# Performance work log

Measured on AMD Instinct MI355X. Metric: run time of the kernel, lower is better.

Reference implementation:

```python
import jax, jax.numpy as jnp
import numpy as np
import math

V, D, H, F, L, S, B = 50257, 1024, 16, 4096, 4, 2048, 2
DK = D // H

def setup_inputs() -> dict:
    key = jax.random.key(0)
    ks = iter(jax.random.split(key, 32))
    std = 0.02
    def nrm(shape):
        return (std * jax.random.normal(next(ks), shape)).astype(jnp.float32)
    inp = {
        "x": jax.random.randint(next(ks), (B, S), 0, V, dtype=jnp.int32),
        "emb": nrm((V, D)),
        "ln1_g": jnp.ones((L, D), jnp.float32), "ln1_b": jnp.zeros((L, D), jnp.float32),
        "wq": nrm((L, D, D)), "wk": nrm((L, D, D)), "wv": nrm((L, D, D)), "wo": nrm((L, D, D)),
        "ln2_g": jnp.ones((L, D), jnp.float32), "ln2_b": jnp.zeros((L, D), jnp.float32),
        "w1": nrm((L, D, F)), "b1": jnp.zeros((L, F), jnp.float32),
        "w2": nrm((L, F, D)), "b2": jnp.zeros((L, D), jnp.float32),
        "lnf_g": jnp.ones((D,), jnp.float32), "lnf_b": jnp.zeros((D,), jnp.float32),
        "head_w": nrm((D, V)), "head_b": jnp.zeros((V,), jnp.float32),
    }
    return inp

def _layernorm(x, g, b, eps=1e-5):
    mu = jnp.mean(x, axis=-1, keepdims=True)
    var = jnp.var(x, axis=-1, keepdims=True)
    return (x - mu) * jax.lax.rsqrt(var + eps) * g + b

def _posenc(seq_len, d_model, dtype):
    pos = jnp.arange(seq_len, dtype=jnp.float32)[:, None]                  # [S,1]
    div = jnp.exp(jnp.arange(0, d_model, 2, dtype=jnp.float32) * (-math.log(10000.0) / d_model))
    ang = pos * div                                                        # [S,D/2]
    pe = jnp.stack([jnp.sin(ang), jnp.cos(ang)], axis=-1).reshape(seq_len, d_model)
    return pe.astype(dtype)

def reference(x, emb, ln1_g, ln1_b, wq, wk, wv, wo, ln2_g, ln2_b, w1, b1, w2, b2, lnf_g, lnf_b, head_w, head_b):
    b, s = x.shape
    h = emb[x] + _posenc(s, D, emb.dtype)[None]                            # [B,S,D]
    causal = jnp.tril(jnp.ones((s, s), dtype=bool))                       # True = keep
    scale = 1.0 / math.sqrt(DK)
    neg_inf = jnp.finfo(h.dtype).min
    for l in range(L):
        # --- attention sublayer ---
        hn = _layernorm(h, ln1_g[l], ln1_b[l])
        q = (hn @ wq[l]).reshape(b, s, H, DK)
        k = (hn @ wk[l]).reshape(b, s, H, DK)
        v = (hn @ wv[l]).reshape(b, s, H, DK)
        scores = jnp.einsum("bqhd,bkhd->bhqk", q, k) * scale
        scores = jnp.where(causal[None, None], scores, neg_inf)
        w = jax.nn.softmax(scores, axis=-1)
        attn = jnp.einsum("bhqk,bkhd->bqhd", w, v).reshape(b, s, D)
        h = h + attn @ wo[l]
        # --- FFN sublayer ---
        hn = _layernorm(h, ln2_g[l], ln2_b[l])
        h = h + jax.nn.relu(hn @ w1[l] + b1[l]) @ w2[l] + b2[l]
    h = _layernorm(h, lnf_g, lnf_b)
    logits = h @ head_w + head_b                                           # [B,S,V]
    return logits
```

## Files before the change

kernel.cpp:

```cpp
#include <hip/hip_runtime.h>
#include <math.h>

#define VOCAB 50257
#define VPAD  50432
#define DM    1024
#define NH    16
#define DKH   64
#define FF    4096
#define NL    4
#define SEQ   2048
#define BATCH 2
#define MROWS (BATCH*SEQ)

typedef __bf16 bf16_t;
typedef __bf16 bf16x8 __attribute__((ext_vector_type(8)));
typedef __bf16 bf16x4 __attribute__((ext_vector_type(4)));
typedef float  f32x4  __attribute__((ext_vector_type(4)));

typedef void as1_void __attribute__((address_space(1)));
typedef void as3_void __attribute__((address_space(3)));

__device__ __forceinline__ void gload_lds16(const void* g, void* l) {
  __builtin_amdgcn_global_load_lds((as1_void*)g, (as3_void*)l, 16, 0, 0);
}

__device__ __forceinline__ uint32_t lds_addr32(const void* p) {
  return (uint32_t)(uintptr_t)(as3_void*)p;
}

__device__ __forceinline__ bf16x8 dsr128(uint32_t addr) {
  bf16x8 v;
  asm volatile("ds_read_b128 %0, %1" : "=v"(v) : "v"(addr));
  return v;
}

#define FENCE asm volatile("" ::: "memory")
#define BAR() do { FENCE; __builtin_amdgcn_s_barrier(); FENCE; } while (0)
#define LGKM0_FENCE() do { \
  asm volatile("s_waitcnt lgkmcnt(0)" ::: "memory"); \
  __builtin_amdgcn_sched_barrier(0); \
} while (0)

__global__ __launch_bounds__(256) void embed_kernel(const int* __restrict__ x,
    const float* __restrict__ emb, float* __restrict__ h) {
  int row = blockIdx.x;
  int s = row & (SEQ - 1);
  int d = threadIdx.x * 4;
  const float* e = emb + (size_t)x[row] * DM + d;
  float4 v = *(const float4*)e;
  float vin[4] = {v.x, v.y, v.z, v.w};
  float out[4];
#pragma unroll
  for (int j = 0; j < 4; ++j) {
    int dd = d + j;
    int i = dd >> 1;
    float freq = expf(-0.017988946039016376f * (float)i);
    float ang = (float)s * freq;
    float pe = (dd & 1) ? cosf(ang) : sinf(ang);
    out[j] = vin[j] + pe;
  }
  *(float4*)(h + (size_t)row * DM + d) = make_float4(out[0], out[1], out[2], out[3]);
}

__global__ __launch_bounds__(256) void ln_kernel(const float* __restrict__ x,
    const float* __restrict__ g, const float* __restrict__ b, bf16_t* __restrict__ out) {
  int row = blockIdx.x;
  int tid = threadIdx.x, lane = tid & 63, wave = tid >> 6;
  const float* xr = x + (size_t)row * DM;
  float4 v = ((const float4*)xr)[tid];
  float s1 = v.x + v.y + v.z + v.w;
  float s2 = v.x * v.x + v.y * v.y + v.z * v.z + v.w * v.w;
#pragma unroll
  for (int d = 1; d < 64; d <<= 1) { s1 += __shfl_xor(s1, d); s2 += __shfl_xor(s2, d); }
  __shared__ float red[8];
  if (lane == 0) { red[wave] = s1; red[4 + wave] = s2; }
  __syncthreads();
  s1 = red[0] + red[1] + red[2] + red[3];
  s2 = red[4] + red[5] + red[6] + red[7];
  float mu = s1 * (1.0f / DM);
  float var = s2 * (1.0f / DM) - mu * mu;
  float rs = rsqrtf(var + 1e-5f);
  float4 gv = ((const float4*)g)[tid];
  float4 bv = ((const float4*)b)[tid];
  bf16x4 o;
  o[0] = (bf16_t)((v.x - mu) * rs * gv.x + bv.x);
  o[1] = (bf16_t)((v.y - mu) * rs * gv.y + bv.y);
  o[2] = (bf16_t)((v.z - mu) * rs * gv.z + bv.z);
  o[3] = (bf16_t)((v.w - mu) * rs * gv.w + bv.w);
  *(bf16x4*)(out + (size_t)row * DM + tid * 4) = o;
}

__global__ __launch_bounds__(256) void transpose_cast_kernel(const float* __restrict__ in,
    bf16_t* __restrict__ out, int K, int N, int Npad) {
  __shared__ float tile[32][33];
  int n0 = blockIdx.x * 32, k0 = blockIdx.y * 32;
  int tx = threadIdx.x & 31, ty = threadIdx.x >> 5;
#pragma unroll
  for (int kk = ty; kk < 32; kk += 8) {
    int n = n0 + tx;
    tile[kk][tx] = (n < N) ? in[(size_t)(k0 + kk) * N + n] : 0.f;
  }
  __syncthreads();
#pragma unroll
  for (int nn = ty; nn < 32; nn += 8) {
    out[(size_t)(n0 + nn) * K + k0 + tx] = (bf16_t)tile[tx][nn];
  }
}

__global__ __launch_bounds__(256) void wtrans_kernel(
    const float* __restrict__ wq, const float* __restrict__ wk,
    const float* __restrict__ wv, const float* __restrict__ wo,
    const float* __restrict__ w1, const float* __restrict__ w2,
    bf16_t* __restrict__ qkvT, bf16_t* __restrict__ woT,
    bf16_t* __restrict__ w1T, bf16_t* __restrict__ w2T) {
  int id = blockIdx.x;
  const float* src; bf16_t* dst; int K, N, tk, tn;
  if (id < 4096) {
    int m = id >> 10, tile_i = id & 1023;
    tk = tile_i >> 5; tn = tile_i & 31; K = 1024; N = 1024;
    src = (m == 0) ? wq : (m == 1) ? wk : (m == 2) ? wv : wo;
    dst = (m < 3) ? qkvT + (size_t)m * DM * DM : woT;
  } else if (id < 8192) {
    int tile_i = id - 4096;
    tk = tile_i >> 7; tn = tile_i & 127; K = 1024; N = 4096;
    src = w1; dst = w1T;
  } else {
    int tile_i = id - 8192;
    tk = tile_i >> 5; tn = tile_i & 31; K = 4096; N = 1024;
    src = w2; dst = w2T;
  }
  __shared__ float tile[32][33];
  int n0 = tn * 32, k0 = tk * 32;
  int tx = threadIdx.x & 31, ty = threadIdx.x >> 5;
#pragma unroll
  for (int kk = ty; kk < 32; kk += 8)
    tile[kk][tx] = src[(size_t)(k0 + kk) * N + n0 + tx];
  __syncthreads();
#pragma unroll
  for (int nn = ty; nn < 32; nn += 8)
    dst[(size_t)(n0 + nn) * K + k0 + tx] = (bf16_t)tile[tx][nn];
}

__global__ __launch_bounds__(256) void vtrans_kernel(const bf16_t* __restrict__ qkv,
    bf16_t* __restrict__ vT) {
  int sb = blockIdx.x, hh = blockIdx.y, bb = blockIdx.z;
  __shared__ bf16_t t[64][72];
  int tid = threadIdx.x;
  const bf16_t* src = qkv + ((size_t)bb * SEQ + sb * 64) * (3 * DM) + 2 * DM + hh * DKH;
#pragma unroll
  for (int c = 0; c < 2; ++c) {
    int u = c * 256 + tid;
    int s = u >> 3, d8 = u & 7;
    *(bf16x8*)&t[s][d8 * 8] = *(const bf16x8*)(src + (size_t)s * (3 * DM) + d8 * 8);
  }
  __syncthreads();
  bf16_t* dst = vT + ((size_t)(bb * NH + hh) * DKH) * SEQ + sb * 64;
#pragma unroll
  for (int c = 0; c < 2; ++c) {
    int u = c * 256 + tid;
    int dk = u >> 3, s8 = u & 7;
    bf16x8 v;
#pragma unroll
    for (int j = 0; j < 8; ++j) v[j] = t[s8 * 8 + j][dk];
    *(bf16x8*)(dst + (size_t)dk * SEQ + s8 * 8) = v;
  }
}

__global__ __launch_bounds__(256, 2) void gemm128_kernel(
    const bf16_t* __restrict__ A, const bf16_t* __restrict__ Bt, int K,
    const float* __restrict__ bias, const float* __restrict__ Rsd,
    float* Cf, bf16_t* Cb, int ldc, int Nvalid, int relu, int gridM, int gridN) {
  __shared__ __align__(16) bf16_t lds[32768];

  int nwg = gridM * gridN;
  int orig = blockIdx.x;
  int q = nwg >> 3, rr = nwg & 7;
  int xcd = orig & 7, idx = orig >> 3;
  int swz = (xcd < rr ? xcd * (q + 1) : rr * (q + 1) + (xcd - rr) * q) + idx;
  int bm = swz % gridM, bn = swz / gridM;
  int m0 = bm * 128, n0 = bn * 128;

  int tid = threadIdx.x, lane = tid & 63, wave = tid >> 6;
  int g = lane >> 4, r = lane & 15;
  int wr = wave >> 1, wc = wave & 1;

  f32x4 zero = {0.f, 0.f, 0.f, 0.f};
  f32x4 acc[4][4];
#pragma unroll
  for (int i = 0; i < 4; ++i)
#pragma unroll
    for (int j = 0; j < 4; ++j) acc[i][j] = zero;

  const bf16_t* Abase = A + (size_t)m0 * K;
  const bf16_t* Bbase = Bt + (size_t)n0 * K;
  int NT = K >> 6;

  uint32_t L0 = lds_addr32(lds);
  uint32_t aF = L0 + (uint32_t)((g * 128 + wr * 64 + r) * 16);
  uint32_t bF = L0 + 32768u + (uint32_t)((g * 128 + wc * 64 + r) * 16);

  auto stage = [&](int t) {
    int b = t & 1, k0 = t << 6;
    bf16_t* dA = lds + (size_t)b * 8192;
    bf16_t* dB = lds + 16384 + (size_t)b * 8192;
#pragma unroll
    for (int j = 0; j < 4; ++j) {
      int u = j * 256 + tid;
      int row = u & 127, k8 = u >> 7;
      gload_lds16(Abase + (size_t)row * K + k0 + k8 * 8, dA + (j * 256 + wave * 64) * 8);
    }
#pragma unroll
    for (int j = 0; j < 4; ++j) {
      int u = j * 256 + tid;
      int row = u & 127, k8 = u >> 7;
      gload_lds16(Bbase + (size_t)row * K + k0 + k8 * 8, dB + (j * 256 + wave * 64) * 8);
    }
  };

  stage(0);
  if (NT > 1) {
    stage(1);
    asm volatile("s_waitcnt vmcnt(8)" ::: "memory");
  } else {
    asm volatile("s_waitcnt vmcnt(0)" ::: "memory");
  }
  BAR();

  for (int t = 0; t < NT; ++t) {
    uint32_t boff = (uint32_t)((t & 1) << 14);
    bf16x8 af[4][2], bfr[4][2];
#pragma unroll
    for (int mr = 0; mr < 4; ++mr)
#pragma unroll
      for (int kk = 0; kk < 2; ++kk)
        af[mr][kk] = dsr128(aF + boff + (uint32_t)(kk * 8192 + mr * 256));
#pragma unroll
    for (int nr = 0; nr < 4; ++nr)
#pragma unroll
      for (int kk = 0; kk < 2; ++kk)
        bfr[nr][kk] = dsr128(bF + boff + (uint32_t)(kk * 8192 + nr * 256));
    LGKM0_FENCE();
    BAR();
    if (t + 2 < NT) stage(t + 2);
    __builtin_amdgcn_s_setprio(1);
#pragma unroll
    for (int mr = 0; mr < 4; ++mr)
#pragma unroll
      for (int nr = 0; nr < 4; ++nr) {
        acc[mr][nr] = __builtin_amdgcn_mfma_f32_16x16x32_bf16(af[mr][0], bfr[nr][0], acc[mr][nr], 0, 0, 0);
        acc[mr][nr] = __builtin_amdgcn_mfma_f32_16x16x32_bf16(af[mr][1], bfr[nr][1], acc[mr][nr], 0, 0, 0);
      }
    __builtin_amdgcn_s_setprio(0);
    __builtin_amdgcn_sched_barrier(0);
    if (t + 2 < NT) {
      asm volatile("s_waitcnt vmcnt(8)" ::: "memory");
    } else {
      asm volatile("s_waitcnt vmcnt(0)" ::: "memory");
    }
    BAR();
  }

#pragma unroll
  for (int mr = 0; mr < 4; ++mr) {
    int row = m0 + wr * 64 + mr * 16 + g * 4;
#pragma unroll
    for (int nr = 0; nr < 4; ++nr) {
      int col = n0 + wc * 64 + nr * 16 + r;
      if (col < Nvalid) {
        float bval = bias ? bias[col] : 0.f;
#pragma unroll
        for (int i = 0; i < 4; ++i) {
          float vv = acc[mr][nr][i] + bval;
          if (relu) vv = fmaxf(vv, 0.f);
          size_t idxo = (size_t)(row + i) * ldc + col;
          if (Rsd) vv += Rsd[idxo];
          if (Cf) Cf[idxo] = vv;
          if (Cb) Cb[idxo] = (bf16_t)vv;
        }
      }
    }
  }
}

__global__ __launch_bounds__(512, 2) void gemm256_kernel(
    const bf16_t* __restrict__ A, const bf16_t* __restrict__ Bt, int K,
    const float* __restrict__ bias, float* Cf, bf16_t* Cb,
    int ldc, int Nvalid, int relu, int gridM, int gridN) {
  __shared__ __align__(16) bf16_t lds[65536];

  int nwg = gridM * gridN;
  int orig = blockIdx.x;
  int q = nwg >> 3, rr = nwg & 7;
  int xcd = orig & 7, idx = orig >> 3;
  int swz = (xcd < rr ? xcd * (q + 1) : rr * (q + 1) + (xcd - rr) * q) + idx;
  int bm = swz % gridM, bn = swz / gridM;
  int m0 = bm * 256, n0 = bn * 256;

  int tid = threadIdx.x, lane = tid & 63, wave = tid >> 6;
  int g = lane >> 4, r = lane & 15;
  int wr = wave >> 2, wc = wave & 3;

  f32x4 zero = {0.f, 0.f, 0.f, 0.f};
  f32x4 acc[8][4];
#pragma unroll
  for (int i = 0; i < 8; ++i)
#pragma unroll
    for (int j = 0; j < 4; ++j) acc[i][j] = zero;

  const bf16_t* Ab = A + (size_t)m0 * K;
  const bf16_t* Bb = Bt + (size_t)n0 * K;
  int NT = K >> 6;

  uint32_t L0 = lds_addr32(lds);
  uint32_t laneOff = (uint32_t)(g * 2048 + r * 16);
  uint32_t aBase0 = L0 + ((uint32_t)wr << 14) + laneOff;
  uint32_t bBase0 = L0 + 65536u + ((uint32_t)(wc >> 1) << 14) + laneOff
                  + (uint32_t)((wc & 1) * 1024);

  auto stageA = [&](int t, int hh) {
    int b = t & 1, k0 = t << 6;
    const bf16_t* src = Ab + (size_t)(hh * 128) * K + k0;
    bf16_t* dst = lds + (size_t)(b * 2 + hh) * 8192;
#pragma unroll
    for (int j = 0; j < 2; ++j) {
      int u = j * 512 + tid;
      gload_lds16(src + (size_t)(u & 127) * K + (u >> 7) * 8, dst + (j * 512 + wave * 64) * 8);
    }
  };
  auto stageB = [&](int t, int hh) {
    int b = t & 1, k0 = t << 6;
    const bf16_t* src = Bb + (size_t)(hh * 128) * K + k0;
    bf16_t* dst = lds + 32768 + (size_t)(b * 2 + hh) * 8192;
#pragma unroll
    for (int j = 0; j < 2; ++j) {
      int u = j * 512 + tid;
      gload_lds16(src + (size_t)(u & 127) * K + (u >> 7) * 8, dst + (j * 512 + wave * 64) * 8);
    }
  };

  stageB(0, 0); stageB(0, 1); stageA(0, 0); stageA(0, 1);
  if (NT > 1) {
    stageB(1, 0); stageB(1, 1);
    asm volatile("s_waitcnt vmcnt(4)" ::: "memory");
  } else {
    asm volatile("s_waitcnt vmcnt(0)" ::: "memory");
  }
  BAR();

  for (int t = 0; t < NT; ++t) {
    uint32_t bsel = (uint32_t)((t & 1) << 15);
    uint32_t Aaddr = aBase0 + bsel;
    uint32_t Baddr = bBase0 + bsel;

    bf16x8 a0[4][2], a1[4][2], b01[2][2], b23[2][2];

#pragma unroll
    for (int mi = 0; mi < 4; ++mi)
#pragma unroll
      for (int kk = 0; kk < 2; ++kk)
        a0[mi][kk] = dsr128(Aaddr + (uint32_t)(kk * 8192 + mi * 256));
#pragma unroll
    for (int ni = 0; ni < 2; ++ni)
#pragma unroll
      for (int kk = 0; kk < 2; ++kk)
        b01[ni][kk] = dsr128(Baddr + (uint32_t)(kk * 8192 + ni * 256));
    if (t + 1 < NT) stageA(t + 1, 0);
    BAR();
    LGKM0_FENCE();
    __builtin_amdgcn_s_setprio(1);
#pragma unroll
    for (int mi = 0; mi < 4; ++mi)
#pragma unroll
      for (int ni = 0; ni < 2; ++ni)
#pragma unroll
        for (int kk = 0; kk < 2; ++kk)
          acc[mi][ni] = __builtin_amdgcn_mfma_f32_16x16x32_bf16(a0[mi][kk], b01[ni][kk], acc[mi][ni], 0, 0, 0);
    __builtin_amdgcn_s_setprio(0);
    __builtin_amdgcn_sched_barrier(0);
    BAR();

#pragma unroll
    for (int ni = 0; ni < 2; ++ni)
#pragma unroll
      for (int kk = 0; kk < 2; ++kk)
        b23[ni][kk] = dsr128(Baddr + (uint32_t)(kk * 8192 + (ni + 2) * 256));
    if (t + 1 < NT) stageA(t + 1, 1);
    BAR();
    LGKM0_FENCE();
    __builtin_amdgcn_s_setprio(1);
#pragma unroll
    for (int mi = 0; mi < 4; ++mi)
#pragma unroll
      for (int ni = 0; ni < 2; ++ni)
#pragma unroll
        for (int kk = 0; kk < 2; ++kk)
          acc[mi][ni + 2] = __builtin_amdgcn_mfma_f32_16x16x32_bf16(a0[mi][kk], b23[ni][kk], acc[mi][ni + 2], 0, 0, 0);
    __builtin_amdgcn_s_setprio(0);
    __builtin_amdgcn_sched_barrier(0);
    BAR();

#pragma unroll
    for (int mi = 0; mi < 4; ++mi)
#pragma unroll
      for (int kk = 0; kk < 2; ++kk)
        a1[mi][kk] = dsr128(Aaddr + (uint32_t)(kk * 8192 + (mi + 4) * 256));
    if (t + 2 < NT) stageB(t + 2, 0);
    BAR();
    LGKM0_FENCE();
    __builtin_amdgcn_s_setprio(1);
#pragma unroll
    for (int mi = 0; mi < 4; ++mi)
#pragma unroll
      for (int ni = 0; ni < 2; ++ni)
#pragma unroll
        for (int kk = 0; kk < 2; ++kk)
          acc[mi + 4][ni] = __builtin_amdgcn_mfma_f32_16x16x32_bf16(a1[mi][kk], b01[ni][kk], acc[mi + 4][ni], 0, 0, 0);
    __builtin_amdgcn_s_setprio(0);
    __builtin_amdgcn_sched_barrier(0);
    BAR();

    if (t + 2 < NT) stageB(t + 2, 1);
    __builtin_amdgcn_sched_barrier(0);
    __builtin_amdgcn_s_setprio(1);
#pragma unroll
    for (int mi = 0; mi < 4; ++mi)
#pragma unroll
      for (int ni = 0; ni < 2; ++ni)
#pragma unroll
        for (int kk = 0; kk < 2; ++kk)
          acc[mi + 4][ni + 2] = __builtin_amdgcn_mfma_f32_16x16x32_bf16(a1[mi][kk], b23[ni][kk], acc[mi + 4][ni + 2], 0, 0, 0);
    __builtin_amdgcn_s_setprio(0);
    __builtin_amdgcn_sched_barrier(0);
    if (t + 2 < NT) {
      asm volatile("s_waitcnt vmcnt(4)" ::: "memory");
    } else {
      asm volatile("s_waitcnt vmcnt(0)" ::: "memory");
    }
    BAR();
  }

#pragma unroll
  for (int mi = 0; mi < 8; ++mi) {
    int row = m0 + wr * 128 + mi * 16 + g * 4;
#pragma unroll
    for (int ni = 0; ni < 4; ++ni) {
      int col = n0 + wc * 64 + ni * 16 + r;
      if (col < Nvalid) {
        float bval = bias ? bias[col] : 0.f;
#pragma unroll
        for (int i = 0; i < 4; ++i) {
          float vv = acc[mi][ni][i] + bval;
          if (relu) vv = fmaxf(vv, 0.f);
          size_t idxo = (size_t)(row + i) * ldc + col;
          if (Cf) Cf[idxo] = vv;
          if (Cb) Cb[idxo] = (bf16_t)vv;
        }
      }
    }
  }
}

__global__ __launch_bounds__(512, 4) void attn_kernel(const bf16_t* __restrict__ Qg,
    const bf16_t* __restrict__ Kg, const bf16_t* __restrict__ vT, bf16_t* __restrict__ Og,
    int ldq) {
  int bq = (int)gridDim.x - 1 - (int)blockIdx.x;
  int hh = blockIdx.y, bb = blockIdx.z;
  int tid = threadIdx.x, lane = tid & 63, wave = tid >> 6;
  int g = lane >> 4, r = lane & 15;
  __shared__ __align__(16) bf16_t Kl[2][4096];
  __shared__ __align__(16) bf16_t Vl[2][4096];
  __shared__ __align__(16) bf16_t Pl[8][1024];

  size_t base = (size_t)bb * SEQ * ldq + hh * DKH;
  size_t vbase = ((size_t)(bb * NH + hh)) * DKH * SEQ;
  size_t baseO = (size_t)bb * SEQ * DM + hh * DKH;
  int q0 = bq * 128 + wave * 16;
  const bf16_t* qrowp = Qg + base + (size_t)(q0 + r) * ldq;
  bf16x8 qf0 = *(const bf16x8*)(qrowp + g * 8);
  bf16x8 qf1 = *(const bf16x8*)(qrowp + 32 + g * 8);
#pragma unroll
  for (int j = 0; j < 8; ++j) {
    qf0[j] = (bf16_t)((float)qf0[j] * 0.125f);
    qf1[j] = (bf16_t)((float)qf1[j] * 0.125f);
  }

  uint32_t KlA = lds_addr32(&Kl[0][0]);
  uint32_t VlA = lds_addr32(&Vl[0][0]);
  int slot0 = g ^ (r & 7), slot1 = (4 + g) ^ (r & 7);

  f32x4 zero = {0.f, 0.f, 0.f, 0.f};
  f32x4 accO[4];
#pragma unroll
  for (int dt = 0; dt < 4; ++dt) accO[dt] = zero;
  float m_i[4], l_i[4];
#pragma unroll
  for (int i = 0; i < 4; ++i) { m_i[i] = -1e30f; l_i[i] = 0.f; }

  int skv = tid >> 3, kslot = tid & 7, kdk8 = kslot ^ (skv & 7);
  int sdk = tid >> 3, vslot = tid & 7, vkv8 = vslot ^ (sdk & 7);
  const bf16_t* ksrc0 = Kg + base + (size_t)skv * ldq + kdk8 * 8;
  const bf16_t* vsrc0 = vT + vbase + (size_t)sdk * SEQ + vkv8 * 8;

  auto stage = [&](int kb) {
    int c = kb & 1;
    gload_lds16(ksrc0 + (size_t)(kb * 64) * ldq, &Kl[c][(wave * 64) * 8]);
    gload_lds16(vsrc0 + kb * 64, &Vl[c][(wave * 64) * 8]);
  };

  int nkb = 2 * bq + 2;
  stage(0); stage(1);
  asm volatile("s_waitcnt vmcnt(2)" ::: "memory");
  BAR();

  for (int kb = 0; kb < nkb; ++kb) {
    uint32_t koff = KlA + (uint32_t)((kb & 1) << 13);
    uint32_t voff = VlA + (uint32_t)((kb & 1) << 13);

    bf16x8 kf[4][2];
#pragma unroll
    for (int ct = 0; ct < 4; ++ct) {
      int kvrow = ct * 16 + r;
      kf[ct][0] = dsr128(koff + (uint32_t)((kvrow * 8 + slot0) * 16));
      kf[ct][1] = dsr128(koff + (uint32_t)((kvrow * 8 + slot1) * 16));
    }
    LGKM0_FENCE();
    f32x4 sc[4];
#pragma unroll
    for (int ct = 0; ct < 4; ++ct) {
      f32x4 s = zero;
      s = __builtin_amdgcn_mfma_f32_16x16x32_bf16(qf0, kf[ct][0], s, 0, 0, 0);
      s = __builtin_amdgcn_mfma_f32_16x16x32_bf16(qf1, kf[ct][1], s, 0, 0, 0);
      sc[ct] = s;
    }

    bool full = (kb * 64 + 63) <= q0;
#pragma unroll
    for (int i = 0; i < 4; ++i) {
      float mx = m_i[i];
      if (full) {
#pragma unroll
        for (int ct = 0; ct < 4; ++ct) mx = fmaxf(mx, sc[ct][i]);
      } else {
        int qglob = q0 + g * 4 + i;
#pragma unroll
        for (int ct = 0; ct < 4; ++ct) {
          int kglob = kb * 64 + ct * 16 + r;
          float s = (kglob <= qglob) ? sc[ct][i] : -1e30f;
          sc[ct][i] = s;
          mx = fmaxf(mx, s);
        }
      }
#pragma unroll
      for (int d = 1; d < 16; d <<= 1) mx = fmaxf(mx, __shfl_xor(mx, d));
      float scl = __expf(m_i[i] - mx);
      l_i[i] *= scl;
      m_i[i] = mx;
      float rsum = 0.f;
#pragma unroll
      for (int ct = 0; ct < 4; ++ct) {
        float p = __expf(sc[ct][i] - mx);
        sc[ct][i] = p;
        rsum += p;
      }
#pragma unroll
      for (int d = 1; d < 16; d <<= 1) rsum += __shfl_xor(rsum, d);
      l_i[i] += rsum;
#pragma unroll
      for (int dt = 0; dt < 4; ++dt) accO[dt][i] *= scl;
    }

#pragma unroll
    for (int ct = 0; ct < 4; ++ct) {
      int kcol = ct * 16 + r;
#pragma unroll
      for (int i = 0; i < 4; ++i)
        Pl[wave][((kcol >> 3) * 16 + g * 4 + i) * 8 + (kcol & 7)] = (bf16_t)sc[ct][i];
    }
    bf16x8 pa0 = *(const bf16x8*)&Pl[wave][((0 + g) * 16 + r) * 8];
    bf16x8 pa1 = *(const bf16x8*)&Pl[wave][((4 + g) * 16 + r) * 8];

    bf16x8 vb[4][2];
#pragma unroll
    for (int dt = 0; dt < 4; ++dt) {
      int dkrow = dt * 16 + r;
      vb[dt][0] = dsr128(voff + (uint32_t)((dkrow * 8 + slot0) * 16));
      vb[dt][1] = dsr128(voff + (uint32_t)((dkrow * 8 + slot1) * 16));
    }
    LGKM0_FENCE();
#pragma unroll
    for (int dt = 0; dt < 4; ++dt) {
      accO[dt] = __builtin_amdgcn_mfma_f32_16x16x32_bf16(pa0, vb[dt][0], accO[dt], 0, 0, 0);
      accO[dt] = __builtin_amdgcn_mfma_f32_16x16x32_bf16(pa1, vb[dt][1], accO[dt], 0, 0, 0);
    }

    BAR();
    if (kb + 2 < nkb) {
      stage(kb + 2);
      asm volatile("s_waitcnt vmcnt(2)" ::: "memory");
    } else {
      asm volatile("s_waitcnt vmcnt(0)" ::: "memory");
    }
    BAR();
  }

#pragma unroll
  for (int dt = 0; dt < 4; ++dt)
#pragma unroll
    for (int i = 0; i < 4; ++i) {
      int rowq = q0 + g * 4 + i;
      Og[baseO + (size_t)rowq * DM + dt * 16 + r] = (bf16_t)(accO[dt][i] / l_i[i]);
    }
}

static inline void launch_gemm256(const bf16_t* A, const bf16_t* Bt, int K,
    const float* bias, float* Cf, bf16_t* Cb, int ldc, int Nvalid, int relu,
    int M, int Npad, hipStream_t stream) {
  int gridM = M / 256, gridN = Npad / 256;
  gemm256_kernel<<<dim3(gridM * gridN), 512, 0, stream>>>(
      A, Bt, K, bias, Cf, Cb, ldc, Nvalid, relu, gridM, gridN);
}

static inline void launch_gemm128(const bf16_t* A, const bf16_t* Bt, int K,
    const float* bias, const float* Rsd, float* Cf, bf16_t* Cb,
    int ldc, int Nvalid, int relu, int M, int Npad, hipStream_t stream) {
  int gridM = M / 128, gridN = Npad / 128;
  gemm128_kernel<<<dim3(gridM * gridN), 256, 0, stream>>>(
      A, Bt, K, bias, Rsd, Cf, Cb, ldc, Nvalid, relu, gridM, gridN);
}

extern "C" void kernel_launch(void* const* d_in, const int* in_sizes, int n_in,
                              void* d_out, int out_size, void* d_ws, size_t ws_size,
                              hipStream_t stream) {
  const int*   x      = (const int*)d_in[0];
  const float* emb    = (const float*)d_in[1];
  const float* ln1_g  = (const float*)d_in[2];
  const float* ln1_b  = (const float*)d_in[3];
  const float* wq     = (const float*)d_in[4];
  const float* wk     = (const float*)d_in[5];
  const float* wv     = (const float*)d_in[6];
  const float* wo     = (const float*)d_in[7];
  const float* ln2_g  = (const float*)d_in[8];
  const float* ln2_b  = (const float*)d_in[9];
  const float* w1     = (const float*)d_in[10];
  const float* b1     = (const float*)d_in[11];
  const float* w2     = (const float*)d_in[12];
  const float* b2     = (const float*)d_in[13];
  const float* lnf_g  = (const float*)d_in[14];
  const float* lnf_b  = (const float*)d_in[15];
  const float* head_w = (const float*)d_in[16];
  const float* head_b = (const float*)d_in[17];
  float* out = (float*)d_out;

  char* ws = (char*)d_ws;
  size_t off = 0;
  auto alloc = [&](size_t bytes) -> void* {
    void* p = ws + off;
    off += (bytes + 255) & ~(size_t)255;
    return p;
  };
  float*  h     = (float*)alloc((size_t)MROWS * DM * 4);
  bf16_t* hn    = (bf16_t*)alloc((size_t)MROWS * DM * 2);
  bf16_t* qkv   = (bf16_t*)alloc((size_t)MROWS * 3 * DM * 2);
  bf16_t* atb   = (bf16_t*)alloc((size_t)MROWS * DM * 2);
  bf16_t* ffn1  = (bf16_t*)alloc((size_t)MROWS * FF * 2);
  bf16_t* vTb   = (bf16_t*)alloc((size_t)BATCH * NH * DKH * SEQ * 2);
  bf16_t* headT = (bf16_t*)alloc((size_t)VPAD * DM * 2);
  bf16_t* wqkvT = headT;
  bf16_t* woT   = headT + (size_t)3 * DM * DM;
  bf16_t* w1T   = headT + (size_t)4 * DM * DM;
  bf16_t* w2T   = headT + (size_t)4 * DM * DM + (size_t)DM * FF;

  embed_kernel<<<MROWS, 256, 0, stream>>>(x, emb, h);

  for (int l = 0; l < NL; ++l) {
    ln_kernel<<<MROWS, 256, 0, stream>>>(h, ln1_g + l * DM, ln1_b + l * DM, hn);

    wtrans_kernel<<<12288, 256, 0, stream>>>(
        wq + (size_t)l * DM * DM, wk + (size_t)l * DM * DM, wv + (size_t)l * DM * DM,
        wo + (size_t)l * DM * DM, w1 + (size_t)l * DM * FF, w2 + (size_t)l * FF * DM,
        wqkvT, woT, w1T, w2T);

    launch_gemm256(hn, wqkvT, DM, nullptr, nullptr, qkv, 3 * DM, 3 * DM, 0,
                   MROWS, 3 * DM, stream);

    vtrans_kernel<<<dim3(SEQ / 64, NH, BATCH), 256, 0, stream>>>(qkv, vTb);
    attn_kernel<<<dim3(SEQ / 128, NH, BATCH), 512, 0, stream>>>(
        qkv, qkv + DM, vTb, atb, 3 * DM);

    launch_gemm128(atb, woT, DM, nullptr, h, h, nullptr, DM, DM, 0, MROWS, DM, stream);

    ln_kernel<<<MROWS, 256, 0, stream>>>(h, ln2_g + l * DM, ln2_b + l * DM, hn);

    launch_gemm256(hn, w1T, DM, b1 + (size_t)l * FF, nullptr, ffn1, FF, FF, 1,
                   MROWS, FF, stream);

    launch_gemm128(ffn1, w2T, FF, b2 + (size_t)l * DM, h, h, nullptr, DM, DM, 0,
                   MROWS, DM, stream);
  }

  ln_kernel<<<MROWS, 256, 0, stream>>>(h, lnf_g, lnf_b, hn);
  transpose_cast_kernel<<<dim3(VPAD / 32, DM / 32), 256, 0, stream>>>(
      head_w, headT, DM, VOCAB, VPAD);
  launch_gemm256(hn, headT, DM, head_b, out, nullptr, VOCAB, VOCAB, 0,
                 MROWS, VPAD, stream);
}
```

Baseline: 2.260 ms.

## Software-pipeline LDS fragment reads one phase ahead of MFMA in GEMM loop

Restructures the GEMM main loop so LDS fragment reads for the next phase (and the first phase of the next k-tile) are issued before the current MFMA block runs. Partial lgkmcnt waits replace full waits, and two barriers per iteration are removed. The aim is to hide LDS read latency behind matrix-core work and cut barrier stalls. It costs more live registers and depends on barrier and waitcnt ordering being correct for the double-buffered LDS, which could race or lower occupancy.

```diff
diff --git a/kernel.cpp b/kernel.cpp
--- a/kernel.cpp
+++ b/kernel.cpp
@@ -36,10 +36,11 @@
 
 #define FENCE asm volatile("" ::: "memory")
 #define BAR() do { FENCE; __builtin_amdgcn_s_barrier(); FENCE; } while (0)
-#define LGKM0_FENCE() do { \
-  asm volatile("s_waitcnt lgkmcnt(0)" ::: "memory"); \
+#define LGKM_FENCE(n) do { \
+  asm volatile("s_waitcnt lgkmcnt(" #n ")" ::: "memory"); \
   __builtin_amdgcn_sched_barrier(0); \
 } while (0)
+#define LGKM0_FENCE() LGKM_FENCE(0)
 
 __global__ __launch_bounds__(256) void embed_kernel(const int* __restrict__ x,
     const float* __restrict__ emb, float* __restrict__ h) {
@@ -347,26 +348,35 @@
   }
   BAR();
 
+  bf16x8 a0[4][2], a1[4][2], b01[2][2], b23[2][2];
+#pragma unroll
+  for (int mi = 0; mi < 4; ++mi)
+#pragma unroll
+    for (int kk = 0; kk < 2; ++kk)
+      a0[mi][kk] = dsr128(aBase0 + (uint32_t)(kk * 8192 + mi * 256));
+#pragma unroll
+  for (int ni = 0; ni < 2; ++ni)
+#pragma unroll
+    for (int kk = 0; kk < 2; ++kk)
+      b01[ni][kk] = dsr128(bBase0 + (uint32_t)(kk * 8192 + ni * 256));
+  __builtin_amdgcn_sched_barrier(0);
+
   for (int t = 0; t < NT; ++t) {
     uint32_t bsel = (uint32_t)((t & 1) << 15);
     uint32_t Aaddr = aBase0 + bsel;
     uint32_t Baddr = bBase0 + bsel;
-
-    bf16x8 a0[4][2], a1[4][2], b01[2][2], b23[2][2];
-
-#pragma unroll
-    for (int mi = 0; mi < 4; ++mi)
+    uint32_t bseln = (uint32_t)(((t + 1) & 1) << 15);
+    uint32_t AaddrN = aBase0 + bseln;
+    uint32_t BaddrN = bBase0 + bseln;
+
+#pragma unroll
+    for (int ni = 0; ni < 2; ++ni)
 #pragma unroll
       for (int kk = 0; kk < 2; ++kk)
-        a0[mi][kk] = dsr128(Aaddr + (uint32_t)(kk * 8192 + mi * 256));
-#pragma unroll
-    for (int ni = 0; ni < 2; ++ni)
-#pragma unroll
-      for (int kk = 0; kk < 2; ++kk)
-        b01[ni][kk] = dsr128(Baddr + (uint32_t)(kk * 8192 + ni * 256));
+        b23[ni][kk] = dsr128(Baddr + (uint32_t)(kk * 8192 + (ni + 2) * 256));
+    __builtin_amdgcn_sched_barrier(0);
     if (t + 1 < NT) stageA(t + 1, 0);
-    BAR();
-    LGKM0_FENCE();
+    LGKM_FENCE(4);
     __builtin_amdgcn_s_setprio(1);
 #pragma unroll
     for (int mi = 0; mi < 4; ++mi)
@@ -380,13 +390,13 @@
     BAR();
 
 #pragma unroll
-    for (int ni = 0; ni < 2; ++ni)
+    for (int mi = 0; mi < 4; ++mi)
 #pragma unroll
       for (int kk = 0; kk < 2; ++kk)
-        b23[ni][kk] = dsr128(Baddr + (uint32_t)(kk * 8192 + (ni + 2) * 256));
+        a1[mi][kk] = dsr128(Aaddr + (uint32_t)(kk * 8192 + (mi + 4) * 256));
+    __builtin_amdgcn_sched_barrier(0);
     if (t + 1 < NT) stageA(t + 1, 1);
-    BAR();
-    LGKM0_FENCE();
+    LGKM_FENCE(8);
     __builtin_amdgcn_s_setprio(1);
 #pragma unroll
     for (int mi = 0; mi < 4; ++mi)
@@ -399,14 +409,8 @@
     __builtin_amdgcn_sched_barrier(0);
     BAR();
 
-#pragma unroll
-    for (int mi = 0; mi < 4; ++mi)
-#pragma unroll
-      for (int kk = 0; kk < 2; ++kk)
-        a1[mi][kk] = dsr128(Aaddr + (uint32_t)(kk * 8192 + (mi + 4) * 256));
     if (t + 2 < NT) stageB(t + 2, 0);
-    BAR();
-    LGKM0_FENCE();
+    LGKM_FENCE(0);
     __builtin_amdgcn_s_setprio(1);
 #pragma unroll
     for (int mi = 0; mi < 4; ++mi)
@@ -419,8 +423,26 @@
     __builtin_amdgcn_sched_barrier(0);
     BAR();
 
-    if (t + 2 < NT) stageB(t + 2, 1);
-    __builtin_amdgcn_sched_barrier(0);
+    if (t + 2 < NT) {
+      stageB(t + 2, 1);
+      asm volatile("s_waitcnt vmcnt(4)" ::: "memory");
+    } else {
+      asm volatile("s_waitcnt vmcnt(0)" ::: "memory");
+    }
+    BAR();
+    if (t + 1 < NT) {
+#pragma unroll
+      for (int mi = 0; mi < 4; ++mi)
+#pragma unroll
+        for (int kk = 0; kk < 2; ++kk)
+          a0[mi][kk] = dsr128(AaddrN + (uint32_t)(kk * 8192 + mi * 256));
+#pragma unroll
+      for (int ni = 0; ni < 2; ++ni)
+#pragma unroll
+        for (int kk = 0; kk < 2; ++kk)
+          b01[ni][kk] = dsr128(BaddrN + (uint32_t)(kk * 8192 + ni * 256));
+      __builtin_amdgcn_sched_barrier(0);
+    }
     __builtin_amdgcn_s_setprio(1);
 #pragma unroll
     for (int mi = 0; mi < 4; ++mi)
@@ -431,12 +453,6 @@
           acc[mi + 4][ni + 2] = __builtin_amdgcn_mfma_f32_16x16x32_bf16(a1[mi][kk], b23[ni][kk], acc[mi + 4][ni + 2], 0, 0, 0);
     __builtin_amdgcn_s_setprio(0);
     __builtin_amdgcn_sched_barrier(0);
-    if (t + 2 < NT) {
-      asm volatile("s_waitcnt vmcnt(4)" ::: "memory");
-    } else {
-      asm volatile("s_waitcnt vmcnt(0)" ::: "memory");
-    }
-    BAR();
   }
 
 #pragma unroll
```

Result: no change. 2.260 ms (+0.0%).

## Switch GEMM pipelines to 4-stage ring with 32-wide K tiles

Applied to the files above, without the earlier changes.

Both GEMM kernels (128x128 and 256x256) now stage K in chunks of 32 instead of 64, using a 4-slot LDS ring buffer with three tiles in flight. This replaces the 2-stage double buffer and its multiple barriers per iteration. The 256 kernel's four-phase interleaved schedule is simplified to a single load-then-MFMA phase with one barrier per K step. The goal is deeper prefetch to hide global latency and fewer sync points, at the cost of twice as many loop iterations and less MFMA work between barriers.

```diff
diff --git a/kernel.cpp b/kernel.cpp
--- a/kernel.cpp
+++ b/kernel.cpp
@@ -39,6 +39,11 @@
 #define LGKM0_FENCE() do { \
   asm volatile("s_waitcnt lgkmcnt(0)" ::: "memory"); \
   __builtin_amdgcn_sched_barrier(0); \
+} while (0)
+#define VMCNT_CHAIN(t, NT, n2, n1) do { \
+  if ((t) + 3 < (NT))      asm volatile("s_waitcnt vmcnt(" #n2 ")" ::: "memory"); \
+  else if ((t) + 2 < (NT)) asm volatile("s_waitcnt vmcnt(" #n1 ")" ::: "memory"); \
+  else                     asm volatile("s_waitcnt vmcnt(0)" ::: "memory"); \
 } while (0)
 
 __global__ __launch_bounds__(256) void embed_kernel(const int* __restrict__ x,
@@ -193,24 +198,24 @@
 
   const bf16_t* Abase = A + (size_t)m0 * K;
   const bf16_t* Bbase = Bt + (size_t)n0 * K;
-  int NT = K >> 6;
+  int NT = K >> 5;
 
   uint32_t L0 = lds_addr32(lds);
-  uint32_t aF = L0 + (uint32_t)((g * 128 + wr * 64 + r) * 16);
-  uint32_t bF = L0 + 32768u + (uint32_t)((g * 128 + wc * 64 + r) * 16);
+  uint32_t aF = L0 + (uint32_t)(g * 2048 + (wr * 64 + r) * 16);
+  uint32_t bF = L0 + 32768u + (uint32_t)(g * 2048 + (wc * 64 + r) * 16);
 
   auto stage = [&](int t) {
-    int b = t & 1, k0 = t << 6;
-    bf16_t* dA = lds + (size_t)b * 8192;
-    bf16_t* dB = lds + 16384 + (size_t)b * 8192;
-#pragma unroll
-    for (int j = 0; j < 4; ++j) {
+    int b = t & 3, k0 = t << 5;
+    bf16_t* dA = lds + (size_t)b * 4096;
+    bf16_t* dB = lds + 16384 + (size_t)b * 4096;
+#pragma unroll
+    for (int j = 0; j < 2; ++j) {
       int u = j * 256 + tid;
       int row = u & 127, k8 = u >> 7;
       gload_lds16(Abase + (size_t)row * K + k0 + k8 * 8, dA + (j * 256 + wave * 64) * 8);
     }
 #pragma unroll
-    for (int j = 0; j < 4; ++j) {
+    for (int j = 0; j < 2; ++j) {
       int u = j * 256 + tid;
       int row = u & 127, k8 = u >> 7;
       gload_lds16(Bbase + (size_t)row * K + k0 + k8 * 8, dB + (j * 256 + wave * 64) * 8);
@@ -218,45 +223,31 @@
   };
 
   stage(0);
-  if (NT > 1) {
-    stage(1);
-    asm volatile("s_waitcnt vmcnt(8)" ::: "memory");
-  } else {
-    asm volatile("s_waitcnt vmcnt(0)" ::: "memory");
-  }
+  if (NT > 1) stage(1);
+  if (NT > 2) stage(2);
+  if (NT > 2)      { asm volatile("s_waitcnt vmcnt(8)" ::: "memory"); }
+  else if (NT > 1) { asm volatile("s_waitcnt vmcnt(4)" ::: "memory"); }
+  else             { asm volatile("s_waitcnt vmcnt(0)" ::: "memory"); }
   BAR();
 
   for (int t = 0; t < NT; ++t) {
-    uint32_t boff = (uint32_t)((t & 1) << 14);
-    bf16x8 af[4][2], bfr[4][2];
+    uint32_t bo = (uint32_t)((t & 3) << 13);
+    if (t + 3 < NT) stage(t + 3);
+    bf16x8 af[4], bfr[4];
+#pragma unroll
+    for (int mr = 0; mr < 4; ++mr) af[mr] = dsr128(aF + bo + (uint32_t)(mr * 256));
+#pragma unroll
+    for (int nr = 0; nr < 4; ++nr) bfr[nr] = dsr128(bF + bo + (uint32_t)(nr * 256));
+    LGKM0_FENCE();
+    __builtin_amdgcn_s_setprio(1);
 #pragma unroll
     for (int mr = 0; mr < 4; ++mr)
 #pragma unroll
-      for (int kk = 0; kk < 2; ++kk)
-        af[mr][kk] = dsr128(aF + boff + (uint32_t)(kk * 8192 + mr * 256));
-#pragma unroll
-    for (int nr = 0; nr < 4; ++nr)
-#pragma unroll
-      for (int kk = 0; kk < 2; ++kk)
-        bfr[nr][kk] = dsr128(bF + boff + (uint32_t)(kk * 8192 + nr * 256));
-    LGKM0_FENCE();
-    BAR();
-    if (t + 2 < NT) stage(t + 2);
-    __builtin_amdgcn_s_setprio(1);
-#pragma unroll
-    for (int mr = 0; mr < 4; ++mr)
-#pragma unroll
-      for (int nr = 0; nr < 4; ++nr) {
-        acc[mr][nr] = __builtin_amdgcn_mfma_f32_16x16x32_bf16(af[mr][0], bfr[nr][0], acc[mr][nr], 0, 0, 0);
-        acc[mr][nr] = __builtin_amdgcn_mfma_f32_16x16x32_bf16(af[mr][1], bfr[nr][1], acc[mr][nr], 0, 0, 0);
-      }
+      for (int nr = 0; nr < 4; ++nr)
+        acc[mr][nr] = __builtin_amdgcn_mfma_f32_16x16x32_bf16(af[mr], bfr[nr], acc[mr][nr], 0, 0, 0);
     __builtin_amdgcn_s_setprio(0);
     __builtin_amdgcn_sched_barrier(0);
-    if (t + 2 < NT) {
-      asm volatile("s_waitcnt vmcnt(8)" ::: "memory");
-    } else {
-      asm volatile("s_waitcnt vmcnt(0)" ::: "memory");
-    }
+    VMCNT_CHAIN(t, NT, 8, 4);
     BAR();
   }
 
@@ -309,133 +300,56 @@
 
   const bf16_t* Ab = A + (size_t)m0 * K;
   const bf16_t* Bb = Bt + (size_t)n0 * K;
-  int NT = K >> 6;
+  int NT = K >> 5;
 
   uint32_t L0 = lds_addr32(lds);
-  uint32_t laneOff = (uint32_t)(g * 2048 + r * 16);
-  uint32_t aBase0 = L0 + ((uint32_t)wr << 14) + laneOff;
-  uint32_t bBase0 = L0 + 65536u + ((uint32_t)(wc >> 1) << 14) + laneOff
-                  + (uint32_t)((wc & 1) * 1024);
-
-  auto stageA = [&](int t, int hh) {
-    int b = t & 1, k0 = t << 6;
-    const bf16_t* src = Ab + (size_t)(hh * 128) * K + k0;
-    bf16_t* dst = lds + (size_t)(b * 2 + hh) * 8192;
+  uint32_t aF = L0 + (uint32_t)(g * 4096 + (wr * 128 + r) * 16);
+  uint32_t bF = L0 + 65536u + (uint32_t)(g * 4096 + (wc * 64 + r) * 16);
+
+  auto stage = [&](int t) {
+    int b = t & 3, k0 = t << 5;
+    bf16_t* dA = lds + (size_t)b * 8192;
+    bf16_t* dB = lds + 32768 + (size_t)b * 8192;
 #pragma unroll
     for (int j = 0; j < 2; ++j) {
       int u = j * 512 + tid;
-      gload_lds16(src + (size_t)(u & 127) * K + (u >> 7) * 8, dst + (j * 512 + wave * 64) * 8);
-    }
-  };
-  auto stageB = [&](int t, int hh) {
-    int b = t & 1, k0 = t << 6;
-    const bf16_t* src = Bb + (size_t)(hh * 128) * K + k0;
-    bf16_t* dst = lds + 32768 + (size_t)(b * 2 + hh) * 8192;
+      int row = u & 255, k8 = u >> 8;
+      gload_lds16(Ab + (size_t)row * K + k0 + k8 * 8, dA + (j * 512 + wave * 64) * 8);
+    }
 #pragma unroll
     for (int j = 0; j < 2; ++j) {
       int u = j * 512 + tid;
-      gload_lds16(src + (size_t)(u & 127) * K + (u >> 7) * 8, dst + (j * 512 + wave * 64) * 8);
+      int row = u & 255, k8 = u >> 8;
+      gload_lds16(Bb + (size_t)row * K + k0 + k8 * 8, dB + (j * 512 + wave * 64) * 8);
     }
   };
 
-  stageB(0, 0); stageB(0, 1); stageA(0, 0); stageA(0, 1);
-  if (NT > 1) {
-    stageB(1, 0); stageB(1, 1);
-    asm volatile("s_waitcnt vmcnt(4)" ::: "memory");
-  } else {
-    asm volatile("s_waitcnt vmcnt(0)" ::: "memory");
-  }
+  stage(0);
+  if (NT > 1) stage(1);
+  if (NT > 2) stage(2);
+  if (NT > 2)      { asm volatile("s_waitcnt vmcnt(8)" ::: "memory"); }
+  else if (NT > 1) { asm volatile("s_waitcnt vmcnt(4)" ::: "memory"); }
+  else             { asm volatile("s_waitcnt vmcnt(0)" ::: "memory"); }
   BAR();
 
   for (int t = 0; t < NT; ++t) {
-    uint32_t bsel = (uint32_t)((t & 1) << 15);
-    uint32_t Aaddr = aBase0 + bsel;
-    uint32_t Baddr = bBase0 + bsel;
-
-    bf16x8 a0[4][2], a1[4][2], b01[2][2], b23[2][2];
-
-#pragma unroll
-    for (int mi = 0; mi < 4; ++mi)
-#pragma unroll
-      for (int kk = 0; kk < 2; ++kk)
-        a0[mi][kk] = dsr128(Aaddr + (uint32_t)(kk * 8192 + mi * 256));
-#pragma unroll
-    for (int ni = 0; ni < 2; ++ni)
-#pragma unroll
-      for (int kk = 0; kk < 2; ++kk)
-        b01[ni][kk] = dsr128(Baddr + (uint32_t)(kk * 8192 + ni * 256));
-    if (t + 1 < NT) stageA(t + 1, 0);
-    BAR();
+    uint32_t bo = (uint32_t)((t & 3) << 14);
+    if (t + 3 < NT) stage(t + 3);
+    bf16x8 af[8], bfr[4];
+#pragma unroll
+    for (int mi = 0; mi < 8; ++mi) af[mi] = dsr128(aF + bo + (uint32_t)(mi * 256));
+#pragma unroll
+    for (int ni = 0; ni < 4; ++ni) bfr[ni] = dsr128(bF + bo + (uint32_t)(ni * 256));
     LGKM0_FENCE();
     __builtin_amdgcn_s_setprio(1);
 #pragma unroll
-    for (int mi = 0; mi < 4; ++mi)
-#pragma unroll
-      for (int ni = 0; ni < 2; ++ni)
-#pragma unroll
-        for (int kk = 0; kk < 2; ++kk)
-          acc[mi][ni] = __builtin_amdgcn_mfma_f32_16x16x32_bf16(a0[mi][kk], b01[ni][kk], acc[mi][ni], 0, 0, 0);
+    for (int mi = 0; mi < 8; ++mi)
+#pragma unroll
+      for (int ni = 0; ni < 4; ++ni)
+        acc[mi][ni] = __builtin_amdgcn_mfma_f32_16x16x32_bf16(af[mi], bfr[ni], acc[mi][ni], 0, 0, 0);
     __builtin_amdgcn_s_setprio(0);
     __builtin_amdgcn_sched_barrier(0);
-    BAR();
-
-#pragma unroll
-    for (int ni = 0; ni < 2; ++ni)
-#pragma unroll
-      for (int kk = 0; kk < 2; ++kk)
-        b23[ni][kk] = dsr128(Baddr + (uint32_t)(kk * 8192 + (ni + 2) * 256));
-    if (t + 1 < NT) stageA(t + 1, 1);
-    BAR();
-    LGKM0_FENCE();
-    __builtin_amdgcn_s_setprio(1);
-#pragma unroll
-    for (int mi = 0; mi < 4; ++mi)
-#pragma unroll
-      for (int ni = 0; ni < 2; ++ni)
-#pragma unroll
-        for (int kk = 0; kk < 2; ++kk)
-          acc[mi][ni + 2] = __builtin_amdgcn_mfma_f32_16x16x32_bf16(a0[mi][kk], b23[ni][kk], acc[mi][ni + 2], 0, 0, 0);
-    __builtin_amdgcn_s_setprio(0);
-    __builtin_amdgcn_sched_barrier(0);
-    BAR();
-
-#pragma unroll
-    for (int mi = 0; mi < 4; ++mi)
-#pragma unroll
-      for (int kk = 0; kk < 2; ++kk)
-        a1[mi][kk] = dsr128(Aaddr + (uint32_t)(kk * 8192 + (mi + 4) * 256));
-    if (t + 2 < NT) stageB(t + 2, 0);
-    BAR();
-    LGKM0_FENCE();
-    __builtin_amdgcn_s_setprio(1);
-#pragma unroll
-    for (int mi = 0; mi < 4; ++mi)
-#pragma unroll
-      for (int ni = 0; ni < 2; ++ni)
-#pragma unroll
-        for (int kk = 0; kk < 2; ++kk)
-          acc[mi + 4][ni] = __builtin_amdgcn_mfma_f32_16x16x32_bf16(a1[mi][kk], b01[ni][kk], acc[mi + 4][ni], 0, 0, 0);
-    __builtin_amdgcn_s_setprio(0);
-    __builtin_amdgcn_sched_barrier(0);
-    BAR();
-
-    if (t + 2 < NT) stageB(t + 2, 1);
-    __builtin_amdgcn_sched_barrier(0);
-    __builtin_amdgcn_s_setprio(1);
-#pragma unroll
-    for (int mi = 0; mi < 4; ++mi)
-#pragma unroll
-      for (int ni = 0; ni < 2; ++ni)
-#pragma unroll
-        for (int kk = 0; kk < 2; ++kk)
-          acc[mi + 4][ni + 2] = __builtin_amdgcn_mfma_f32_16x16x32_bf16(a1[mi][kk], b23[ni][kk], acc[mi + 4][ni + 2], 0, 0, 0);
-    __builtin_amdgcn_s_setprio(0);
-    __builtin_amdgcn_sched_barrier(0);
-    if (t + 2 < NT) {
-      asm volatile("s_waitcnt vmcnt(4)" ::: "memory");
-    } else {
-      asm volatile("s_waitcnt vmcnt(0)" ::: "memory");
-    }
+    VMCNT_CHAIN(t, NT, 8, 4);
     BAR();
   }
 
```

New measurement: 2.517 ms. 11.4% more time.

## Add dedicated 128x256-tile GEMM with XCD swizzle for LM head

Applied to the files above, without the earlier changes.

Replaces the generic 256-tile GEMM for the vocabulary projection with a specialized kernel that uses 128x256 tiles, K-step 32 double-buffered LDS loads via global_load_lds, and a workgroup-index remap that groups tiles by XCD for L2 locality. Smaller per-block register footprint allows more occupancy (launch bounds 512,4) and a larger grid for the output-store-heavy head GEMM. It risks lower arithmetic intensity per tile and more reloads of A/B.

```diff
diff --git a/kernel.cpp b/kernel.cpp
--- a/kernel.cpp
+++ b/kernel.cpp
@@ -454,6 +454,109 @@
           size_t idxo = (size_t)(row + i) * ldc + col;
           if (Cf) Cf[idxo] = vv;
           if (Cb) Cb[idxo] = (bf16_t)vv;
+        }
+      }
+    }
+  }
+}
+
+__global__ __launch_bounds__(512, 4) void gemmhd_kernel(
+    const bf16_t* __restrict__ A, const bf16_t* __restrict__ Bt, int K,
+    const float* __restrict__ bias, float* __restrict__ Cf,
+    int ldc, int Nvalid, int gridM, int gridN) {
+  __shared__ __align__(16) bf16_t lds[24576];
+
+  int nwg = gridM * gridN;
+  int orig = blockIdx.x;
+  int q = nwg >> 3, rr = nwg & 7;
+  int xcd = orig & 7, idx = orig >> 3;
+  int swz = (xcd < rr ? xcd * (q + 1) : rr * (q + 1) + (xcd - rr) * q) + idx;
+  int bm = swz % gridM, bn = swz / gridM;
+  int m0 = bm * 128, n0 = bn * 256;
+
+  int tid = threadIdx.x, lane = tid & 63, wave = tid >> 6;
+  int g = lane >> 4, r = lane & 15;
+  int wr = wave >> 2, wc = wave & 3;
+
+  f32x4 zero = {0.f, 0.f, 0.f, 0.f};
+  f32x4 acc[4][4];
+#pragma unroll
+  for (int i = 0; i < 4; ++i)
+#pragma unroll
+    for (int j = 0; j < 4; ++j) acc[i][j] = zero;
+
+  const bf16_t* Abase = A + (size_t)m0 * K;
+  const bf16_t* Bbase = Bt + (size_t)n0 * K;
+  int NT = K >> 5;
+
+  uint32_t L0 = lds_addr32(lds);
+  uint32_t aF = L0 + (uint32_t)(g * 2048 + (wr * 64 + r) * 16);
+  uint32_t bF = L0 + 16384u + (uint32_t)(g * 4096 + (wc * 64 + r) * 16);
+
+  auto stage = [&](int t) {
+    int b = t & 1, k0 = t << 5;
+    bf16_t* dA = lds + (size_t)b * 4096;
+    bf16_t* dB = lds + 8192 + (size_t)b * 8192;
+    {
+      int u = tid;
+      int row = u & 127, k8 = u >> 7;
+      gload_lds16(Abase + (size_t)row * K + k0 + k8 * 8, dA + (wave * 64) * 8);
+    }
+#pragma unroll
+    for (int j = 0; j < 2; ++j) {
+      int u = j * 512 + tid;
+      int row = u & 255, k8 = u >> 8;
+      gload_lds16(Bbase + (size_t)row * K + k0 + k8 * 8, dB + (j * 512 + wave * 64) * 8);
+    }
+  };
+
+  stage(0);
+  if (NT > 1) {
+    stage(1);
+    asm volatile("s_waitcnt vmcnt(3)" ::: "memory");
+  } else {
+    asm volatile("s_waitcnt vmcnt(0)" ::: "memory");
+  }
+  BAR();
+
+  for (int t = 0; t < NT; ++t) {
+    uint32_t aoff = (uint32_t)((t & 1) << 13);
+    uint32_t boff = (uint32_t)((t & 1) << 14);
+    bf16x8 af[4], bfr[4];
+#pragma unroll
+    for (int mr = 0; mr < 4; ++mr) af[mr] = dsr128(aF + aoff + (uint32_t)(mr * 256));
+#pragma unroll
+    for (int nr = 0; nr < 4; ++nr) bfr[nr] = dsr128(bF + boff + (uint32_t)(nr * 256));
+    LGKM0_FENCE();
+    BAR();
+    if (t + 2 < NT) stage(t + 2);
+    __builtin_amdgcn_s_setprio(1);
+#pragma unroll
+    for (int mr = 0; mr < 4; ++mr)
+#pragma unroll
+      for (int nr = 0; nr < 4; ++nr)
+        acc[mr][nr] = __builtin_amdgcn_mfma_f32_16x16x32_bf16(af[mr], bfr[nr], acc[mr][nr], 0, 0, 0);
+    __builtin_amdgcn_s_setprio(0);
+    __builtin_amdgcn_sched_barrier(0);
+    if (t + 2 < NT) {
+      asm volatile("s_waitcnt vmcnt(3)" ::: "memory");
+    } else {
+      asm volatile("s_waitcnt vmcnt(0)" ::: "memory");
+    }
+    BAR();
+  }
+
+#pragma unroll
+  for (int mr = 0; mr < 4; ++mr) {
+    int row = m0 + wr * 64 + mr * 16 + g * 4;
+#pragma unroll
+    for (int nr = 0; nr < 4; ++nr) {
+      int col = n0 + wc * 64 + nr * 16 + r;
+      if (col < Nvalid) {
+        float bval = bias ? bias[col] : 0.f;
+#pragma unroll
+        for (int i = 0; i < 4; ++i) {
+          Cf[(size_t)(row + i) * ldc + col] = acc[mr][nr][i] + bval;
         }
       }
     }
@@ -701,6 +804,6 @@
   ln_kernel<<<MROWS, 256, 0, stream>>>(h, lnf_g, lnf_b, hn);
   transpose_cast_kernel<<<dim3(VPAD / 32, DM / 32), 256, 0, stream>>>(
       head_w, headT, DM, VOCAB, VPAD);
-  launch_gemm256(hn, headT, DM, head_b, out, nullptr, VOCAB, VOCAB, 0,
-                 MROWS, VPAD, stream);
-}
+  gemmhd_kernel<<<dim3((MROWS / 128) * (VPAD / 256)), 512, 0, stream>>>(
+      hn, headT, DM, head_b, out, VOCAB, VOCAB, MROWS / 128, VPAD / 256);
+}
```

After: 2.473 ms. 1.09x slower.
